# Kernel optimization log

Hardware: AMD Instinct MI355X
Metric: run time of the kernel (lower is better)

Reference implementation:

```python
import jax, jax.numpy as jnp
import numpy as np

EPS = 1e-6
EMBED_DIM = 2048
NUM_HEADS = 16
HEAD_DIM = EMBED_DIM // NUM_HEADS


def setup_inputs() -> dict:
    key = jax.random.key(0)
    ks = jax.random.split(key, 6)
    B, S = 8, 2048
    inputs = jax.random.normal(ks[0], (B, S, EMBED_DIM), dtype=jnp.float32)
    # per-head q/k/v projections, stacked over heads: (H, d, d), no bias (use_bias=False)
    scale = 1.0 / np.sqrt(HEAD_DIM)
    Wq = jax.random.normal(ks[1], (NUM_HEADS, HEAD_DIM, HEAD_DIM), dtype=jnp.float32) * scale
    Wk = jax.random.normal(ks[2], (NUM_HEADS, HEAD_DIM, HEAD_DIM), dtype=jnp.float32) * scale
    Wv = jax.random.normal(ks[3], (NUM_HEADS, HEAD_DIM, HEAD_DIM), dtype=jnp.float32) * scale
    # output projection Dense(embed_dim) with bias (keras default)
    Wo = jax.random.normal(ks[4], (EMBED_DIM, EMBED_DIM), dtype=jnp.float32) / np.sqrt(EMBED_DIM)
    bo = jnp.zeros((EMBED_DIM,), dtype=jnp.float32)
    return {"inputs": inputs, "Wq": Wq, "Wk": Wk, "Wv": Wv, "Wo": Wo, "bo": bo}


def _phi(x):
    # elu(x) + 1 feature map (standard kernelized linear attention)
    return jax.nn.elu(x) + 1.0


def reference(inputs, Wq, Wk, Wv, Wo, bo):
    B, S, E = inputs.shape
    H, d = NUM_HEADS, HEAD_DIM
    # split heads: (B, S, E) -> (B, H, S, d)
    xh = inputs.reshape(B, S, H, d).transpose(0, 2, 1, 3)
    # per-head q/k/v projections, batched over all heads in one einsum each
    q = jnp.einsum('bhsd,hde->bhse', xh, Wq)
    k = jnp.einsum('bhsd,hde->bhse', xh, Wk)
    v = jnp.einsum('bhsd,hde->bhse', xh, Wv)
    pq, pk = _phi(q), _phi(k)
    # non-causal linear attention: out = phi(q) @ (phi(k)^T v) / (phi(q) @ sum phi(k))
    kv = jnp.einsum('bhsd,bhse->bhde', pk, v)          # (B,H,d,d)
    ksum = pk.sum(axis=2)                               # (B,H,d)
    num = jnp.einsum('bhsd,bhde->bhse', pq, kv)         # (B,H,S,d)
    den = jnp.einsum('bhsd,bhd->bhs', pq, ksum)         # (B,H,S)
    ctx = num / (den[..., None] + EPS)
    # combine heads: (B,H,S,d) -> (B,S,E), then output projection
    combined = ctx.transpose(0, 2, 1, 3).reshape(B, S, E)
    return combined @ Wo + bo
```

## Files before the change

### kernel.cpp

```cpp
#include <hip/hip_runtime.h>
#include <stdint.h>

typedef unsigned short u16;
typedef __attribute__((ext_vector_type(4))) float f32x4;
typedef __attribute__((ext_vector_type(8))) __bf16 bf16x8;
typedef __attribute__((ext_vector_type(8))) u16 u16x8;
typedef __attribute__((ext_vector_type(4))) u16 u16x4;

#define AS1 __attribute__((address_space(1)))
#define AS3 __attribute__((address_space(3)))

__device__ __forceinline__ void gload16(const void* g, void* l) {
  __builtin_amdgcn_global_load_lds((const AS1 void*)g, (AS3 void*)l, 16, 0, 0);
}

__device__ __forceinline__ float bf2f(u16 u) {
  union { uint32_t i; float f; } v; v.i = ((uint32_t)u) << 16; return v.f;
}
__device__ __forceinline__ u16 f2bf(float f) {
  uint32_t x = __builtin_bit_cast(uint32_t, f);
  x += 0x7fffu + ((x >> 16) & 1u);
  return (u16)(x >> 16);
}
__device__ __forceinline__ float phi_f(float x) { return x > 0.f ? x + 1.f : __expf(x); }

__device__ __forceinline__ f32x4 mfma16(bf16x8 a, bf16x8 b, f32x4 c) {
  return __builtin_amdgcn_mfma_f32_16x16x32_bf16(a, b, c, 0, 0, 0);
}

__device__ __forceinline__ int permrow(int r) {
  return (r & ~63) | (((r & 3) << 4) + ((r & 63) >> 2));
}

#define OFF_WQT  0ULL
#define OFF_WKT  (OFF_WQT + 524288ULL)
#define OFF_WVT  (OFF_WKT + 524288ULL)
#define OFF_WOT  (OFF_WVT + 524288ULL)
#define OFF_PQ   (OFF_WOT + 8388608ULL)
#define OFF_PKT  (OFF_PQ  + 67108864ULL)
#define OFF_VT   (OFF_PKT + 67108864ULL)
#define OFF_KVP  (OFF_VT  + 67108864ULL)
#define OFF_KVT  (OFF_KVP + 33554432ULL)
#define OFF_KSUM (OFF_KVT + 4194304ULL)
#define OFF_CTX  OFF_PKT
#define WS_NEED  (OFF_KSUM + 65536ULL)

__global__ __launch_bounds__(256) void mla_transpose_cvt(const float* __restrict__ src,
                                                         u16* __restrict__ dst, int n) {
  __shared__ u16 tile[32][33];
  const int b = blockIdx.z;
  const float* s = src + (size_t)b * n * n;
  u16* d = dst + (size_t)b * n * n;
  const int x = blockIdx.x * 32 + threadIdx.x;
  const int y0 = blockIdx.y * 32 + threadIdx.y;
  #pragma unroll
  for (int i = 0; i < 32; i += 8)
    tile[threadIdx.y + i][threadIdx.x] = f2bf(s[(size_t)(y0 + i) * n + x]);
  __syncthreads();
  const int x2 = blockIdx.y * 32 + threadIdx.x;
  const int y2 = blockIdx.x * 32 + threadIdx.y;
  #pragma unroll
  for (int i = 0; i < 32; i += 8) {
    int pr = permrow(y2 + i);
    d[(size_t)pr * n + x2] = tile[threadIdx.x][threadIdx.y + i];
  }
}

__global__ __launch_bounds__(256) void mla_qkv(
    const float* __restrict__ X, const u16* __restrict__ WqT,
    const u16* __restrict__ WkT, const u16* __restrict__ WvT,
    u16* __restrict__ pq, u16* __restrict__ pkT, u16* __restrict__ vT) {
  __shared__ u16 ldsX[128 * 128];
  __shared__ u16 ldsW[128 * 128];
  const int t = threadIdx.x;
  const int rt = blockIdx.x, h = blockIdx.y;
  const int r0 = rt * 128;
  const int b = r0 >> 11;
  const int sl0 = r0 & 2047;
  const int bh = b * 16 + h;
  const u16* Wsrc[3] = { WqT + h * 16384, WkT + h * 16384, WvT + h * 16384 };

  #pragma unroll
  for (int i = 0; i < 8; ++i)
    gload16(Wsrc[0] + i * 2048 + t * 8, &ldsW[i * 2048 + t * 8]);

  const float* Xg = X + (size_t)r0 * 2048 + h * 128;
  #pragma unroll
  for (int j = 0; j < 8; ++j) {
    int e = j * 2048 + t * 8;
    int row = e >> 7, col = e & 127;
    const float* p = Xg + (size_t)row * 2048 + col;
    f32x4 a = *(const f32x4*)p;
    f32x4 c = *(const f32x4*)(p + 4);
    u16x8 wv;
    #pragma unroll
    for (int q = 0; q < 4; ++q) { wv[q] = f2bf(a[q]); wv[4 + q] = f2bf(c[q]); }
    *(u16x8*)&ldsX[permrow(row) * 128 + col] = wv;
  }
  __syncthreads();

  const int wave = t >> 6, lane = t & 63;
  const int wm = (wave >> 1) * 64, wn = (wave & 1) * 64;
  const int lr = lane & 15, lk = (lane >> 4) * 8, r4 = (lane >> 4) * 4;
  const int rainv0 = (lr & 3) * 16 + (lr >> 2);

  for (int wsel = 0; wsel < 3; ++wsel) {
    if (wsel) {
      __syncthreads();
      #pragma unroll
      for (int i = 0; i < 8; ++i)
        gload16(Wsrc[wsel] + i * 2048 + t * 8, &ldsW[i * 2048 + t * 8]);
      __syncthreads();
    }
    f32x4 acc[4][4];
    #pragma unroll
    for (int mb = 0; mb < 4; ++mb)
      #pragma unroll
      for (int nb = 0; nb < 4; ++nb) acc[mb][nb] = (f32x4)0.f;

    if (wsel == 0) {
      #pragma unroll
      for (int ks = 0; ks < 4; ++ks) {
        bf16x8 af[4], bb[4];
        #pragma unroll
        for (int mb = 0; mb < 4; ++mb)
          af[mb] = *(const bf16x8*)&ldsX[(wm + rainv0 + mb * 4) * 128 + ks * 32 + lk];
        #pragma unroll
        for (int nb = 0; nb < 4; ++nb)
          bb[nb] = *(const bf16x8*)&ldsW[(wn + nb * 16 + lr) * 128 + ks * 32 + lk];
        #pragma unroll
        for (int mb = 0; mb < 4; ++mb)
          #pragma unroll
          for (int nb = 0; nb < 4; ++nb)
            acc[mb][nb] = mfma16(af[mb], bb[nb], acc[mb][nb]);
      }
      u16* outq = pq + (size_t)bh * 262144 + (size_t)sl0 * 128;
      #pragma unroll
      for (int mb = 0; mb < 4; ++mb)
        #pragma unroll
        for (int j = 0; j < 4; ++j) {
          int srow = wm + mb * 16 + r4 + j;
          u16x4 o;
          #pragma unroll
          for (int nb = 0; nb < 4; ++nb) o[nb] = f2bf(phi_f(acc[mb][nb][j]));
          *(u16x4*)&outq[srow * 128 + wn + 4 * lr] = o;
        }
    } else {
      #pragma unroll
      for (int ks = 0; ks < 4; ++ks) {
        bf16x8 af[4], bb[4];
        #pragma unroll
        for (int mb = 0; mb < 4; ++mb)
          af[mb] = *(const bf16x8*)&ldsW[(wm + rainv0 + mb * 4) * 128 + ks * 32 + lk];
        #pragma unroll
        for (int nb = 0; nb < 4; ++nb)
          bb[nb] = *(const bf16x8*)&ldsX[(wn + nb * 16 + lr) * 128 + ks * 32 + lk];
        #pragma unroll
        for (int mb = 0; mb < 4; ++mb)
          #pragma unroll
          for (int nb = 0; nb < 4; ++nb)
            acc[mb][nb] = mfma16(af[mb], bb[nb], acc[mb][nb]);
      }
      u16* outT = (wsel == 1 ? pkT : vT) + (size_t)bh * 262144 + sl0;
      #pragma unroll
      for (int mb = 0; mb < 4; ++mb)
        #pragma unroll
        for (int j = 0; j < 4; ++j) {
          int drow = wm + mb * 16 + r4 + j;
          u16x4 o;
          #pragma unroll
          for (int nb = 0; nb < 4; ++nb) {
            float v0 = acc[mb][nb][j];
            if (wsel == 1) v0 = phi_f(v0);
            o[nb] = f2bf(v0);
          }
          *(u16x4*)&outT[(size_t)drow * 2048 + wn + 4 * lr] = o;
        }
    }
  }
}

__global__ __launch_bounds__(256) void mla_kv(
    const u16* __restrict__ pkT, const u16* __restrict__ vT, float* __restrict__ kvp) {
  __shared__ u16 ldsA[4 * 4096];
  __shared__ u16 ldsB[4 * 4096];
  const int t = threadIdx.x;
  const int bh = blockIdx.x, part = blockIdx.y;
  const int s0 = part * 512;
  const u16* Ag = pkT + (size_t)bh * 262144;
  const u16* Bg = vT + (size_t)bh * 262144;

  const int o0 = t * 16;
  const int row0 = o0 >> 6;
  const int c0 = ((((o0 >> 4) & 3) ^ ((row0 >> 1) & 3)) * 8);

  const int wave = t >> 6, lane = t & 63;
  const int wm = (wave >> 1) * 64, wn = (wave & 1) * 64;
  const int lr = lane & 15, hi = lane >> 4, r4 = (lane >> 4) * 4;

  char* lA = (char*)ldsA;
  char* lB = (char*)ldsB;

#define KV_STAGE(u, slotb) do { const int _sc = s0 + (u) * 32 + c0; \
    gload16(Ag + (size_t)row0 * 2048 + _sc, lA + (slotb) + o0); \
    gload16(Ag + (size_t)(row0 + 64) * 2048 + _sc, lA + (slotb) + o0 + 4096); \
    gload16(Bg + (size_t)row0 * 2048 + _sc, lB + (slotb) + o0); \
    gload16(Bg + (size_t)(row0 + 64) * 2048 + _sc, lB + (slotb) + o0 + 4096); } while (0)

  auto rdA = [&](int slotb, int r) -> bf16x8 {
    int p = (r << 6) + (hi << 4);
    p ^= ((r >> 1) & 3) << 4;
    return *(const bf16x8*)(lA + slotb + p);
  };
  auto rdB = [&](int slotb, int r) -> bf16x8 {
    int p = (r << 6) + (hi << 4);
    p ^= ((r >> 1) & 3) << 4;
    return *(const bf16x8*)(lB + slotb + p);
  };

  f32x4 acc[4][4];
  #pragma unroll
  for (int mb = 0; mb < 4; ++mb)
    #pragma unroll
    for (int nb = 0; nb < 4; ++nb) acc[mb][nb] = (f32x4)0.f;

  KV_STAGE(0, 0); KV_STAGE(1, 8192); KV_STAGE(2, 16384);
  asm volatile("s_waitcnt vmcnt(8)" ::: "memory");
  __builtin_amdgcn_s_barrier();

  bf16x8 af[4], bb[4];
  for (int u = 0; u < 13; ++u) {
    const int sb = (u & 3) * 8192;
    #pragma unroll
    for (int mb = 0; mb < 4; ++mb) af[mb] = rdB(sb, wm + mb * 16 + lr);
    #pragma unroll
    for (int nb = 0; nb < 4; ++nb) bb[nb] = rdA(sb, wn + nb * 16 + lr);
    KV_STAGE(u + 3, ((u + 3) & 3) * 8192);
    __builtin_amdgcn_sched_barrier(0);
    __builtin_amdgcn_s_barrier();
    __builtin_amdgcn_s_setprio(1);
    #pragma unroll
    for (int mb = 0; mb < 4; ++mb)
      #pragma unroll
      for (int nb = 0; nb < 4; ++nb)
        acc[mb][nb] = mfma16(af[mb], bb[nb], acc[mb][nb]);
    __builtin_amdgcn_s_setprio(0);
    asm volatile("s_waitcnt vmcnt(8)" ::: "memory");
    __builtin_amdgcn_s_barrier();
  }
  asm volatile("s_waitcnt vmcnt(0)" ::: "memory");
  __builtin_amdgcn_s_barrier();
  #pragma unroll
  for (int u = 13; u < 16; ++u) {
    const int sb = (u & 3) * 8192;
    #pragma unroll
    for (int mb = 0; mb < 4; ++mb) af[mb] = rdB(sb, wm + mb * 16 + lr);
    #pragma unroll
    for (int nb = 0; nb < 4; ++nb) bb[nb] = rdA(sb, wn + nb * 16 + lr);
    #pragma unroll
    for (int mb = 0; mb < 4; ++mb)
      #pragma unroll
      for (int nb = 0; nb < 4; ++nb)
        acc[mb][nb] = mfma16(af[mb], bb[nb], acc[mb][nb]);
  }
#undef KV_STAGE

  float* op = kvp + ((size_t)part * 128 + bh) * 16384;
  #pragma unroll
  for (int mb = 0; mb < 4; ++mb)
    #pragma unroll
    for (int nb = 0; nb < 4; ++nb)
      #pragma unroll
      for (int j = 0; j < 4; ++j)
        op[(wm + mb * 16 + r4 + j) * 128 + wn + nb * 16 + lr] = acc[mb][nb][j];
}

__global__ __launch_bounds__(256) void mla_kvred_ksum(
    const float* __restrict__ kvp, const u16* __restrict__ pkT,
    u16* __restrict__ kvT, float* __restrict__ ksum) {
  const int bid = (int)blockIdx.x;
  const int t = threadIdx.x;
  if (bid < 1024) {
    const size_t i0 = ((size_t)bid * 256 + t) * 8;
    f32x4 lo = (f32x4)0.f, hi = (f32x4)0.f;
    #pragma unroll
    for (int p = 0; p < 4; ++p) {
      const float* src = kvp + (size_t)p * 2097152 + i0;
      lo += *(const f32x4*)src;
      hi += *(const f32x4*)(src + 4);
    }
    u16x8 o;
    #pragma unroll
    for (int j = 0; j < 4; ++j) { o[j] = f2bf(lo[j]); o[4 + j] = f2bf(hi[j]); }
    *(u16x8*)(kvT + i0) = o;
  } else {
    const int lane = t & 63, wave = t >> 6;
    const int gw = (bid - 1024) * 4 + wave;
    const u16* row = pkT + (size_t)gw * 2048;
    float s = 0.f;
    #pragma unroll
    for (int g = 0; g < 4; ++g) {
      u16x8 v = *(const u16x8*)&row[g * 512 + lane * 8];
      #pragma unroll
      for (int j = 0; j < 8; ++j) s += bf2f(v[j]);
    }
    #pragma unroll
    for (int off = 32; off; off >>= 1) s += __shfl_down(s, off);
    if (lane == 0) ksum[gw] = s;
  }
}

__global__ __launch_bounds__(256) void mla_ctx(
    const u16* __restrict__ pq, const u16* __restrict__ kvT,
    const float* __restrict__ ksum, u16* __restrict__ ctx) {
  __shared__ u16 ldsA[128 * 128];
  __shared__ float ksl[128];
  __shared__ float dls[128];
  const int t = threadIdx.x;
  const int st = blockIdx.x, bh = blockIdx.y;
  const int sl0 = st * 128;
  const u16* Ag = pq + (size_t)bh * 262144 + (size_t)sl0 * 128;
  const u16* Bg = kvT + (size_t)bh * 16384;
  #pragma unroll
  for (int i = 0; i < 8; ++i)
    gload16(Ag + i * 2048 + t * 8, &ldsA[i * 2048 + t * 8]);
  if (t < 128) ksl[t] = ksum[bh * 128 + t];
  __syncthreads();
  const int wave = t >> 6, lane = t & 63;
  const int wm = (wave >> 1) * 64, wn = (wave & 1) * 64;
  const int lr = lane & 15, lk = (lane >> 4) * 8, r4 = (lane >> 4) * 4;
  f32x4 acc[4][4];
  #pragma unroll
  for (int mb = 0; mb < 4; ++mb)
    #pragma unroll
    for (int nb = 0; nb < 4; ++nb) acc[mb][nb] = (f32x4)0.f;
  #pragma unroll
  for (int ks = 0; ks < 4; ++ks) {
    bf16x8 af[4], bb[4];
    #pragma unroll
    for (int mb = 0; mb < 4; ++mb)
      af[mb] = *(const bf16x8*)&ldsA[(wm + mb * 16 + lr) * 128 + ks * 32 + lk];
    #pragma unroll
    for (int nb = 0; nb < 4; ++nb)
      bb[nb] = *(const bf16x8*)(Bg + (wn + 4 * lr + nb) * 128 + ks * 32 + lk);
    #pragma unroll
    for (int mb = 0; mb < 4; ++mb)
      #pragma unroll
      for (int nb = 0; nb < 4; ++nb)
        acc[mb][nb] = mfma16(af[mb], bb[nb], acc[mb][nb]);
  }
  if (t < 128) {
    float s = 0.f;
    #pragma unroll
    for (int g = 0; g < 16; ++g) {
      int blk = (g + t) & 15;
      u16x8 v = *(const u16x8*)&ldsA[t * 128 + blk * 8];
      #pragma unroll
      for (int j = 0; j < 8; ++j) s += bf2f(v[j]) * ksl[blk * 8 + j];
    }
    dls[t] = s + 1e-6f;
  }
  __syncthreads();
  const int b = bh >> 4, h = bh & 15;
  u16* oc = ctx + ((size_t)b * 2048 + sl0) * 2048 + h * 128;
  #pragma unroll
  for (int mb = 0; mb < 4; ++mb)
    #pragma unroll
    for (int j = 0; j < 4; ++j) {
      int srow = wm + mb * 16 + r4 + j;
      u16x4 o;
      #pragma unroll
      for (int nb = 0; nb < 4; ++nb) o[nb] = f2bf(acc[mb][nb][j] / dls[srow]);
      *(u16x4*)&oc[(size_t)srow * 2048 + wn + 4 * lr] = o;
    }
}

__global__ __launch_bounds__(512, 2) void mla_out8(
    const u16* __restrict__ ctx, const u16* __restrict__ WoT,
    const float* __restrict__ bo, float* __restrict__ out) {
  __shared__ u16 ldsA[4 * 8192];
  __shared__ u16 ldsB[4 * 8192];
  const int t = threadIdx.x;
  const int bid = (int)blockIdx.x;
  const int swz = (bid & 7) * 64 + (bid >> 3);
  const int mt = swz >> 3, nt = swz & 7;
  const u16* Ag = ctx + (size_t)mt * 256 * 2048;
  const u16* Bg = WoT + (size_t)nt * 256 * 2048;

  const int o0 = t * 16;
  const int row0 = o0 >> 6;
  const int c0 = ((((o0 >> 4) & 3) ^ ((row0 >> 1) & 3)) * 8);

  const int w = t >> 6, lane = t & 63;
  const int wrow = (w >> 2) * 128;
  const int wcol = (w & 3) * 64;
  const int lr = lane & 15, hi = lane >> 4, r4 = (lane >> 4) * 4;

  f32x4 bocache = *(const f32x4*)&bo[nt * 256 + wcol + 4 * lr];

  char* lA = (char*)ldsA;
  char* lB = (char*)ldsB;

#define STAGE_A(u) do { const int _sl = ((u) & 3) * 16384; \
    gload16(Ag + (size_t)row0 * 2048 + (u) * 32 + c0, lA + _sl + o0); \
    gload16(Ag + (size_t)(row0 + 128) * 2048 + (u) * 32 + c0, lA + _sl + o0 + 8192); } while (0)
#define STAGE_B(u) do { const int _sl = ((u) & 3) * 16384; \
    gload16(Bg + (size_t)row0 * 2048 + (u) * 32 + c0, lB + _sl + o0); \
    gload16(Bg + (size_t)(row0 + 128) * 2048 + (u) * 32 + c0, lB + _sl + o0 + 8192); } while (0)

  auto rdA = [&](int slotb, int r) -> bf16x8 {
    int p = (r << 6) + (hi << 4);
    p ^= ((r >> 1) & 3) << 4;
    return *(const bf16x8*)(lA + slotb + p);
  };
  auto rdB = [&](int slotb, int r) -> bf16x8 {
    int p = (r << 6) + (hi << 4);
    p ^= ((r >> 1) & 3) << 4;
    return *(const bf16x8*)(lB + slotb + p);
  };

  f32x4 acc0[4][4], acc1[4][4];
  #pragma unroll
  for (int mb = 0; mb < 4; ++mb)
    #pragma unroll
    for (int nb = 0; nb < 4; ++nb) { acc0[mb][nb] = (f32x4)0.f; acc1[mb][nb] = (f32x4)0.f; }

  STAGE_A(0); STAGE_B(0); STAGE_A(1); STAGE_B(1); STAGE_A(2); STAGE_B(2);
  asm volatile("s_waitcnt vmcnt(8)" ::: "memory");
  __builtin_amdgcn_s_barrier();

  bf16x8 af[4], bb[4];

  for (int u = 0; u < 61; ++u) {
    const int sb = (u & 3) * 16384;
    #pragma unroll
    for (int nb = 0; nb < 4; ++nb) bb[nb] = rdB(sb, wcol + nb * 16 + lr);
    #pragma unroll
    for (int mb = 0; mb < 4; ++mb) af[mb] = rdA(sb, wrow + mb * 16 + lr);
    STAGE_A(u + 3);
    __builtin_amdgcn_sched_barrier(0);
    __builtin_amdgcn_s_barrier();
    __builtin_amdgcn_s_setprio(1);
    #pragma unroll
    for (int mb = 0; mb < 4; ++mb)
      #pragma unroll
      for (int nb = 0; nb < 4; ++nb)
        acc0[mb][nb] = mfma16(af[mb], bb[nb], acc0[mb][nb]);
    __builtin_amdgcn_s_setprio(0);
    __builtin_amdgcn_s_barrier();
    #pragma unroll
    for (int mb = 0; mb < 4; ++mb) af[mb] = rdA(sb, wrow + 64 + mb * 16 + lr);
    STAGE_B(u + 3);
    __builtin_amdgcn_sched_barrier(0);
    __builtin_amdgcn_s_barrier();
    __builtin_amdgcn_s_setprio(1);
    #pragma unroll
    for (int mb = 0; mb < 4; ++mb)
      #pragma unroll
      for (int nb = 0; nb < 4; ++nb)
        acc1[mb][nb] = mfma16(af[mb], bb[nb], acc1[mb][nb]);
    __builtin_amdgcn_s_setprio(0);
    asm volatile("s_waitcnt vmcnt(8)" ::: "memory");
    __builtin_amdgcn_s_barrier();
  }

  asm volatile("s_waitcnt vmcnt(0)" ::: "memory");
  __builtin_amdgcn_s_barrier();
  #pragma unroll
  for (int u = 61; u < 64; ++u) {
    const int sb = (u & 3) * 16384;
    #pragma unroll
    for (int nb = 0; nb < 4; ++nb) bb[nb] = rdB(sb, wcol + nb * 16 + lr);
    #pragma unroll
    for (int mb = 0; mb < 4; ++mb) af[mb] = rdA(sb, wrow + mb * 16 + lr);
    #pragma unroll
    for (int mb = 0; mb < 4; ++mb)
      #pragma unroll
      for (int nb = 0; nb < 4; ++nb)
        acc0[mb][nb] = mfma16(af[mb], bb[nb], acc0[mb][nb]);
    #pragma unroll
    for (int mb = 0; mb < 4; ++mb) af[mb] = rdA(sb, wrow + 64 + mb * 16 + lr);
    #pragma unroll
    for (int mb = 0; mb < 4; ++mb)
      #pragma unroll
      for (int nb = 0; nb < 4; ++nb)
        acc1[mb][nb] = mfma16(af[mb], bb[nb], acc1[mb][nb]);
  }
#undef STAGE_A
#undef STAGE_B

  const size_t obase = (size_t)(mt * 256 + wrow) * 2048 + nt * 256 + wcol + 4 * lr;
  #pragma unroll
  for (int mb = 0; mb < 4; ++mb)
    #pragma unroll
    for (int j = 0; j < 4; ++j) {
      f32x4 v0, v1;
      #pragma unroll
      for (int nb = 0; nb < 4; ++nb) {
        v0[nb] = acc0[mb][nb][j] + bocache[nb];
        v1[nb] = acc1[mb][nb][j] + bocache[nb];
      }
      *(f32x4*)&out[obase + (size_t)(mb * 16 + r4 + j) * 2048] = v0;
      *(f32x4*)&out[obase + (size_t)(64 + mb * 16 + r4 + j) * 2048] = v1;
    }
}

extern "C" void kernel_launch(void* const* d_in, const int* in_sizes, int n_in,
                              void* d_out, int out_size, void* d_ws, size_t ws_size,
                              hipStream_t stream) {
  (void)in_sizes; (void)n_in; (void)out_size;
  const float* X  = (const float*)d_in[0];
  const float* Wq = (const float*)d_in[1];
  const float* Wk = (const float*)d_in[2];
  const float* Wv = (const float*)d_in[3];
  const float* Wo = (const float*)d_in[4];
  const float* bo = (const float*)d_in[5];
  float* out = (float*)d_out;
  char* ws = (char*)d_ws;
  if (ws_size < WS_NEED) return;

  u16*   wqT  = (u16*)(ws + OFF_WQT);
  u16*   wkT  = (u16*)(ws + OFF_WKT);
  u16*   wvT  = (u16*)(ws + OFF_WVT);
  u16*   woT  = (u16*)(ws + OFF_WOT);
  u16*   pq   = (u16*)(ws + OFF_PQ);
  u16*   pkT  = (u16*)(ws + OFF_PKT);
  u16*   vT   = (u16*)(ws + OFF_VT);
  float* kvp  = (float*)(ws + OFF_KVP);
  u16*   kvT  = (u16*)(ws + OFF_KVT);
  float* ksum = (float*)(ws + OFF_KSUM);
  u16*   ctx  = (u16*)(ws + OFF_CTX);

  dim3 tb(32, 8);
  mla_transpose_cvt<<<dim3(4, 4, 16), tb, 0, stream>>>(Wq, wqT, 128);
  mla_transpose_cvt<<<dim3(4, 4, 16), tb, 0, stream>>>(Wk, wkT, 128);
  mla_transpose_cvt<<<dim3(4, 4, 16), tb, 0, stream>>>(Wv, wvT, 128);
  mla_transpose_cvt<<<dim3(64, 64, 1), tb, 0, stream>>>(Wo, woT, 2048);
  mla_qkv<<<dim3(128, 16), 256, 0, stream>>>(X, wqT, wkT, wvT, pq, pkT, vT);
  mla_kv<<<dim3(128, 4), 256, 0, stream>>>(pkT, vT, kvp);
  mla_kvred_ksum<<<5120, 256, 0, stream>>>(kvp, pkT, kvT, ksum);
  mla_ctx<<<dim3(16, 128), 256, 0, stream>>>(pq, kvT, ksum, ctx);
  mla_out8<<<512, 512, 0, stream>>>(ctx, woT, bo, out);
}
```

Baseline: 408.0 us.

## Restructure QKV projection into LDS-free per-wave tiles with register-held weights

The QKV projection kernel no longer stages X and W tiles through LDS. Each wave now computes one 64x64 output quadrant for one of Q/K/V and loads its weight fragments straight into registers. X is read from global memory, converted to bf16 in registers and fed directly to MFMA. The grid becomes 6144 one-dimensional blocks with an XCD-aware remapping of block ids. This removes LDS traffic and barriers and raises parallelism, but each X row is now read by six waves instead of one block, so global/L2 read traffic goes up.

```diff
diff --git a/kernel.cpp b/kernel.cpp
--- a/kernel.cpp
+++ b/kernel.cpp
@@ -26,6 +26,13 @@
 
 __device__ __forceinline__ f32x4 mfma16(bf16x8 a, bf16x8 b, f32x4 c) {
   return __builtin_amdgcn_mfma_f32_16x16x32_bf16(a, b, c, 0, 0, 0);
+}
+
+__device__ __forceinline__ bf16x8 cvt8(f32x4 a, f32x4 b) {
+  bf16x8 r;
+  #pragma unroll
+  for (int i = 0; i < 4; ++i) { r[i] = (__bf16)a[i]; r[4 + i] = (__bf16)b[i]; }
+  return r;
 }
 
 __device__ __forceinline__ int permrow(int r) {
@@ -70,113 +77,109 @@
     const float* __restrict__ X, const u16* __restrict__ WqT,
     const u16* __restrict__ WkT, const u16* __restrict__ WvT,
     u16* __restrict__ pq, u16* __restrict__ pkT, u16* __restrict__ vT) {
-  __shared__ u16 ldsX[128 * 128];
-  __shared__ u16 ldsW[128 * 128];
   const int t = threadIdx.x;
-  const int rt = blockIdx.x, h = blockIdx.y;
-  const int r0 = rt * 128;
-  const int b = r0 >> 11;
-  const int sl0 = r0 & 2047;
-  const int bh = b * 16 + h;
-  const u16* Wsrc[3] = { WqT + h * 16384, WkT + h * 16384, WvT + h * 16384 };
-
-  #pragma unroll
-  for (int i = 0; i < 8; ++i)
-    gload16(Wsrc[0] + i * 2048 + t * 8, &ldsW[i * 2048 + t * 8]);
-
-  const float* Xg = X + (size_t)r0 * 2048 + h * 128;
-  #pragma unroll
-  for (int j = 0; j < 8; ++j) {
-    int e = j * 2048 + t * 8;
-    int row = e >> 7, col = e & 127;
-    const float* p = Xg + (size_t)row * 2048 + col;
-    f32x4 a = *(const f32x4*)p;
-    f32x4 c = *(const f32x4*)(p + 4);
-    u16x8 wv;
-    #pragma unroll
-    for (int q = 0; q < 4; ++q) { wv[q] = f2bf(a[q]); wv[4 + q] = f2bf(c[q]); }
-    *(u16x8*)&ldsX[permrow(row) * 128 + col] = wv;
-  }
-  __syncthreads();
-
-  const int wave = t >> 6, lane = t & 63;
-  const int wm = (wave >> 1) * 64, wn = (wave & 1) * 64;
-  const int lr = lane & 15, lk = (lane >> 4) * 8, r4 = (lane >> 4) * 4;
-  const int rainv0 = (lr & 3) * 16 + (lr >> 2);
-
-  for (int wsel = 0; wsel < 3; ++wsel) {
-    if (wsel) {
-      __syncthreads();
-      #pragma unroll
-      for (int i = 0; i < 8; ++i)
-        gload16(Wsrc[wsel] + i * 2048 + t * 8, &ldsW[i * 2048 + t * 8]);
-      __syncthreads();
-    }
-    f32x4 acc[4][4];
-    #pragma unroll
-    for (int mb = 0; mb < 4; ++mb)
-      #pragma unroll
-      for (int nb = 0; nb < 4; ++nb) acc[mb][nb] = (f32x4)0.f;
-
-    if (wsel == 0) {
-      #pragma unroll
-      for (int ks = 0; ks < 4; ++ks) {
-        bf16x8 af[4], bb[4];
-        #pragma unroll
-        for (int mb = 0; mb < 4; ++mb)
-          af[mb] = *(const bf16x8*)&ldsX[(wm + rainv0 + mb * 4) * 128 + ks * 32 + lk];
-        #pragma unroll
-        for (int nb = 0; nb < 4; ++nb)
-          bb[nb] = *(const bf16x8*)&ldsW[(wn + nb * 16 + lr) * 128 + ks * 32 + lk];
+  const int lane = t & 63, w = t >> 6;
+  const int bid = (int)blockIdx.x;
+  const int logical = (bid & 7) * 768 + (bid >> 3);
+  const int wi = logical * 4 + w;
+  const int c = wi / 96;
+  const int rem = wi % 96;
+  const int h = rem / 6;
+  const int role = rem % 6;
+  const int p = role >> 1, q2 = role & 1;
+  const int bh = (c >> 5) * 16 + h;
+  const int sl = (c & 31) * 64;
+
+  const int lr = lane & 15, hi = lane >> 4;
+  const int lk = hi * 8, r4 = hi * 4;
+  const int rainv = (lr & 3) * 16 + (lr >> 2);
+
+  const u16* Wsrc[3] = { WqT, WkT, WvT };
+  const u16* Wp = Wsrc[p] + h * 16384 + q2 * 64 * 128;
+
+  bf16x8 wf[4][4];
+  if (p == 0) {
+    #pragma unroll
+    for (int nb = 0; nb < 4; ++nb)
+      #pragma unroll
+      for (int ks = 0; ks < 4; ++ks)
+        wf[nb][ks] = *(const bf16x8*)(Wp + (nb * 16 + lr) * 128 + ks * 32 + lk);
+  } else {
+    #pragma unroll
+    for (int mb = 0; mb < 4; ++mb)
+      #pragma unroll
+      for (int ks = 0; ks < 4; ++ks)
+        wf[mb][ks] = *(const bf16x8*)(Wp + (rainv + mb * 4) * 128 + ks * 32 + lk);
+  }
+
+  f32x4 acc[4][4];
+  #pragma unroll
+  for (int mb = 0; mb < 4; ++mb)
+    #pragma unroll
+    for (int nb = 0; nb < 4; ++nb) acc[mb][nb] = (f32x4)0.f;
+
+  const float* Xb = X + (size_t)(c * 64) * 2048 + h * 128;
+
+  #pragma unroll
+  for (int ks2 = 0; ks2 < 2; ++ks2) {
+    bf16x8 xf[4][2];
+    #pragma unroll
+    for (int f = 0; f < 4; ++f) {
+      const int row = (p == 0) ? (f * 16 + lr) : (4 * lr + f);
+      const float* src = Xb + (size_t)row * 2048 + ks2 * 64 + lk;
+      f32x4 a0 = *(const f32x4*)src;
+      f32x4 a1 = *(const f32x4*)(src + 4);
+      f32x4 b0 = *(const f32x4*)(src + 32);
+      f32x4 b1 = *(const f32x4*)(src + 36);
+      xf[f][0] = cvt8(a0, a1);
+      xf[f][1] = cvt8(b0, b1);
+    }
+    #pragma unroll
+    for (int kk = 0; kk < 2; ++kk) {
+      const int ks = ks2 * 2 + kk;
+      if (p == 0) {
         #pragma unroll
         for (int mb = 0; mb < 4; ++mb)
           #pragma unroll
           for (int nb = 0; nb < 4; ++nb)
-            acc[mb][nb] = mfma16(af[mb], bb[nb], acc[mb][nb]);
-      }
-      u16* outq = pq + (size_t)bh * 262144 + (size_t)sl0 * 128;
-      #pragma unroll
-      for (int mb = 0; mb < 4; ++mb)
-        #pragma unroll
-        for (int j = 0; j < 4; ++j) {
-          int srow = wm + mb * 16 + r4 + j;
-          u16x4 o;
-          #pragma unroll
-          for (int nb = 0; nb < 4; ++nb) o[nb] = f2bf(phi_f(acc[mb][nb][j]));
-          *(u16x4*)&outq[srow * 128 + wn + 4 * lr] = o;
-        }
-    } else {
-      #pragma unroll
-      for (int ks = 0; ks < 4; ++ks) {
-        bf16x8 af[4], bb[4];
-        #pragma unroll
-        for (int mb = 0; mb < 4; ++mb)
-          af[mb] = *(const bf16x8*)&ldsW[(wm + rainv0 + mb * 4) * 128 + ks * 32 + lk];
-        #pragma unroll
-        for (int nb = 0; nb < 4; ++nb)
-          bb[nb] = *(const bf16x8*)&ldsX[(wn + nb * 16 + lr) * 128 + ks * 32 + lk];
+            acc[mb][nb] = mfma16(xf[mb][kk], wf[nb][ks], acc[mb][nb]);
+      } else {
         #pragma unroll
         for (int mb = 0; mb < 4; ++mb)
           #pragma unroll
           for (int nb = 0; nb < 4; ++nb)
-            acc[mb][nb] = mfma16(af[mb], bb[nb], acc[mb][nb]);
+            acc[mb][nb] = mfma16(wf[mb][ks], xf[nb][kk], acc[mb][nb]);
       }
-      u16* outT = (wsel == 1 ? pkT : vT) + (size_t)bh * 262144 + sl0;
-      #pragma unroll
-      for (int mb = 0; mb < 4; ++mb)
+    }
+  }
+
+  if (p == 0) {
+    u16* o = pq + (size_t)bh * 262144 + (size_t)sl * 128 + q2 * 64 + 4 * lr;
+    #pragma unroll
+    for (int mb = 0; mb < 4; ++mb)
+      #pragma unroll
+      for (int j = 0; j < 4; ++j) {
+        u16x4 v;
         #pragma unroll
-        for (int j = 0; j < 4; ++j) {
-          int drow = wm + mb * 16 + r4 + j;
-          u16x4 o;
-          #pragma unroll
-          for (int nb = 0; nb < 4; ++nb) {
-            float v0 = acc[mb][nb][j];
-            if (wsel == 1) v0 = phi_f(v0);
-            o[nb] = f2bf(v0);
-          }
-          *(u16x4*)&outT[(size_t)drow * 2048 + wn + 4 * lr] = o;
+        for (int nb = 0; nb < 4; ++nb) v[nb] = f2bf(phi_f(acc[mb][nb][j]));
+        *(u16x4*)(o + (mb * 16 + r4 + j) * 128) = v;
+      }
+  } else {
+    u16* o = (p == 1 ? pkT : vT) + (size_t)bh * 262144 +
+             (size_t)(q2 * 64) * 2048 + sl + 4 * lr;
+    #pragma unroll
+    for (int mb = 0; mb < 4; ++mb)
+      #pragma unroll
+      for (int j = 0; j < 4; ++j) {
+        u16x4 v;
+        #pragma unroll
+        for (int nb = 0; nb < 4; ++nb) {
+          float x = acc[mb][nb][j];
+          if (p == 1) x = phi_f(x);
+          v[nb] = f2bf(x);
         }
-    }
+        *(u16x4*)(o + (size_t)(mb * 16 + r4 + j) * 2048) = v;
+      }
   }
 }
 
@@ -208,14 +211,14 @@
     gload16(Bg + (size_t)(row0 + 64) * 2048 + _sc, lB + (slotb) + o0 + 4096); } while (0)
 
   auto rdA = [&](int slotb, int r) -> bf16x8 {
-    int p = (r << 6) + (hi << 4);
-    p ^= ((r >> 1) & 3) << 4;
-    return *(const bf16x8*)(lA + slotb + p);
+    int pp = (r << 6) + (hi << 4);
+    pp ^= ((r >> 1) & 3) << 4;
+    return *(const bf16x8*)(lA + slotb + pp);
   };
   auto rdB = [&](int slotb, int r) -> bf16x8 {
-    int p = (r << 6) + (hi << 4);
-    p ^= ((r >> 1) & 3) << 4;
-    return *(const bf16x8*)(lB + slotb + p);
+    int pp = (r << 6) + (hi << 4);
+    pp ^= ((r >> 1) & 3) << 4;
+    return *(const bf16x8*)(lB + slotb + pp);
   };
 
   f32x4 acc[4][4];
@@ -536,7 +539,7 @@
   mla_transpose_cvt<<<dim3(4, 4, 16), tb, 0, stream>>>(Wk, wkT, 128);
   mla_transpose_cvt<<<dim3(4, 4, 16), tb, 0, stream>>>(Wv, wvT, 128);
   mla_transpose_cvt<<<dim3(64, 64, 1), tb, 0, stream>>>(Wo, woT, 2048);
-  mla_qkv<<<dim3(128, 16), 256, 0, stream>>>(X, wqT, wkT, wvT, pq, pkT, vT);
+  mla_qkv<<<6144, 256, 0, stream>>>(X, wqT, wkT, wvT, pq, pkT, vT);
   mla_kv<<<dim3(128, 4), 256, 0, stream>>>(pkT, vT, kvp);
   mla_kvred_ksum<<<5120, 256, 0, stream>>>(kvp, pkT, kvT, ksum);
   mla_ctx<<<dim3(16, 128), 256, 0, stream>>>(pq, kvT, ksum, ctx);
```

Result: slower. 469.4 us (+15.1%).
